# Kernel tuning notes

Hardware: AMD Instinct MI355X
Metric: run time of the kernel (lower is better)

The kernel has to match this reference:

```python
import jax, jax.numpy as jnp
import numpy as np

B, T, C = 8, 1024, 768
H, D = 12, 64  # num_heads, head_size; H*D == C
BLOCK = 1024


def setup_inputs() -> dict:
    key = jax.random.key(0)
    ks = jax.random.split(key, 6)
    s = C ** -0.5  # init scale akin to torch Linear default range
    x = jax.random.normal(ks[0], (B, T, C), dtype=jnp.float32)
    Wq = jax.random.normal(ks[1], (C, H, D), dtype=jnp.float32) * s
    Wk = jax.random.normal(ks[2], (C, H, D), dtype=jnp.float32) * s
    Wv = jax.random.normal(ks[3], (C, H, D), dtype=jnp.float32) * s
    Wp = jax.random.normal(ks[4], (C, C), dtype=jnp.float32) * s
    bp = jax.random.normal(ks[5], (C,), dtype=jnp.float32) * s
    return {"x": x, "Wq": Wq, "Wk": Wk, "Wv": Wv, "Wp": Wp, "bp": bp}


def reference(x, Wq, Wk, Wv, Wp, bp):
    # Fused equivalent of the per-head loop: project all heads at once.
    q = jnp.einsum('btc,chd->bhtd', x, Wq)  # [B,H,T,D]
    k = jnp.einsum('btc,chd->bhtd', x, Wk)
    v = jnp.einsum('btc,chd->bhtd', x, Wv)
    scale = D ** -0.5
    scores = jnp.einsum('bhtd,bhsd->bhts', q, k) * scale  # [B,H,T,T]
    causal = jnp.tril(jnp.ones((T, T), dtype=bool))       # tril mask (T <= block_size)
    scores = jnp.where(causal, scores, jnp.finfo(scores.dtype).min)
    att = jax.nn.softmax(scores, axis=-1)
    # dropout layers are identity in eval mode (deterministic reference)
    out = jnp.einsum('bhts,bhsd->bhtd', att, v)            # [B,H,T,D]
    out = out.transpose(0, 2, 1, 3).reshape(B, T, H * D)   # concat heads -> [B,T,C]
    return out @ Wp.T + bp  # output projection (torch Linear: y = x W^T + b)
```

## Files before the change

kernel.cpp:

```cpp
#include <hip/hip_runtime.h>

#define BB 8
#define TT 1024
#define CC 768
#define HH 12
#define DD 64

typedef float f32x4 __attribute__((ext_vector_type(4)));
typedef short s16x8 __attribute__((ext_vector_type(8)));

#define SCALE2 0.18033688011112042f

__device__ __forceinline__ unsigned short f2bf(float f) {
  unsigned u = __builtin_bit_cast(unsigned, f);
  u += 0x7fffu + ((u >> 16) & 1u);
  return (unsigned short)(u >> 16);
}

#define GLOAD_LDS16(gsrc, ldst)                                                     \
  __builtin_amdgcn_global_load_lds(                                                 \
      (const __attribute__((address_space(1))) void*)(gsrc),                        \
      (__attribute__((address_space(3))) void*)(ldst), 16, 0, 0)

__global__ __launch_bounds__(256) void cast_f32_bf16(const float* __restrict__ src,
                                                     unsigned short* __restrict__ dst,
                                                     int n4) {
  int i = blockIdx.x * 256 + threadIdx.x;
  if (i >= n4) return;
  float4 v = ((const float4*)src)[i];
  ushort4 o;
  o.x = f2bf(v.x); o.y = f2bf(v.y); o.z = f2bf(v.z); o.w = f2bf(v.w);
  ((ushort4*)dst)[i] = o;
}

__global__ __launch_bounds__(256) void transpose_w(const float* __restrict__ Wq,
                                                   const float* __restrict__ Wk,
                                                   const float* __restrict__ Wv,
                                                   unsigned short* __restrict__ WT) {
  __shared__ float tile[32][33];
  int bid = blockIdx.x;
  int which = bid / (24 * 24);
  int rem = bid % (24 * 24);
  int cb = (rem / 24) * 32, nb = (rem % 24) * 32;
  const float* W = (which == 0) ? Wq : (which == 1) ? Wk : Wv;
  int t = threadIdx.x;
  int j = t & 31, i0 = t >> 5;
  #pragma unroll
  for (int rr = 0; rr < 4; ++rr) {
    int i = i0 + rr * 8;
    tile[i][j] = W[(size_t)(cb + i) * CC + nb + j];
  }
  __syncthreads();
  #pragma unroll
  for (int rr = 0; rr < 4; ++rr) {
    int i = i0 + rr * 8;
    WT[(size_t)(which * CC + nb + i) * CC + cb + j] = f2bf(tile[j][i]);
  }
}

__device__ __forceinline__ void gemm_tile(const unsigned short* __restrict__ A,
                                          const unsigned short* __restrict__ BT,
                                          int m0, int n0,
                                          unsigned short* As, unsigned short* Bs,
                                          f32x4 acc[4][4]) {
  const int t = threadIdx.x, lane = t & 63, w = t >> 6;
  const int g = lane >> 4, c = lane & 15;
  const int wr = w >> 1, wc = w & 1;
  const int srow = lane >> 3;
  const int scol = (lane & 7) * 8;
  #pragma unroll 1
  for (int kt = 0; kt < CC; kt += 64) {
    __syncthreads();
    #pragma unroll
    for (int p = 0; p < 4; ++p) {
      int row = p * 32 + w * 8 + srow;
      GLOAD_LDS16(A + (size_t)(m0 + row) * CC + kt + scol, As + (p * 32 + w * 8) * 64);
      GLOAD_LDS16(BT + (size_t)(n0 + row) * CC + kt + scol, Bs + (p * 32 + w * 8) * 64);
    }
    __syncthreads();
    #pragma unroll
    for (int ks = 0; ks < 2; ++ks) {
      s16x8 a[4], b[4];
      #pragma unroll
      for (int i = 0; i < 4; ++i) {
        a[i] = *(const s16x8*)(As + (wr * 64 + i * 16 + c) * 64 + ks * 32 + g * 8);
        b[i] = *(const s16x8*)(Bs + (wc * 64 + i * 16 + c) * 64 + ks * 32 + g * 8);
      }
      #pragma unroll
      for (int i = 0; i < 4; ++i)
        #pragma unroll
        for (int j = 0; j < 4; ++j)
          acc[i][j] = __builtin_amdgcn_mfma_f32_16x16x32_bf16(a[i], b[j], acc[i][j], 0, 0, 0);
    }
  }
}

__global__ __launch_bounds__(256) void gemm_qkv(const unsigned short* __restrict__ xb,
                                                const unsigned short* __restrict__ WT,
                                                unsigned short* __restrict__ qb,
                                                unsigned short* __restrict__ kb,
                                                unsigned short* __restrict__ vT) {
  __shared__ unsigned short As[128 * 64], Bs[128 * 64];
  int bid = blockIdx.x;
  int bm = bid % 64, bn = bid / 64;
  int m0 = bm * 128, n0 = bn * 128;
  f32x4 acc[4][4];
  #pragma unroll
  for (int i = 0; i < 4; ++i)
    #pragma unroll
    for (int j = 0; j < 4; ++j)
      acc[i][j] = (f32x4){0.f, 0.f, 0.f, 0.f};
  gemm_tile(xb, WT, m0, n0, As, Bs, acc);

  const int t = threadIdx.x, lane = t & 63, w = t >> 6;
  const int g = lane >> 4, c = lane & 15;
  const int wr = w >> 1, wc = w & 1;
  #pragma unroll
  for (int i = 0; i < 4; ++i) {
    int mrow = m0 + wr * 64 + i * 16 + g * 4;
    int b = mrow >> 10, tt_ = mrow & 1023;
    #pragma unroll
    for (int j = 0; j < 4; ++j) {
      int nbv = n0 + wc * 64 + j * 16;
      int which = nbv / CC;
      int rm = nbv - which * CC;
      int h = rm >> 6, d0 = rm & 63;
      if (which == 2) {
        ushort4 pk;
        pk.x = f2bf(acc[i][j][0]); pk.y = f2bf(acc[i][j][1]);
        pk.z = f2bf(acc[i][j][2]); pk.w = f2bf(acc[i][j][3]);
        *(ushort4*)(vT + ((size_t)(b * HH + h) * DD + d0 + c) * TT + tt_) = pk;
      } else {
        float sc = which ? 1.0f : SCALE2;
        unsigned short* dst = (which ? kb : qb) +
                              ((size_t)(b * HH + h) * TT + tt_) * DD + d0 + c;
        dst[0]      = f2bf(acc[i][j][0] * sc);
        dst[DD]     = f2bf(acc[i][j][1] * sc);
        dst[2 * DD] = f2bf(acc[i][j][2] * sc);
        dst[3 * DD] = f2bf(acc[i][j][3] * sc);
      }
    }
  }
}

__global__ __launch_bounds__(256, 4) void attn(const unsigned short* __restrict__ qb,
                                               const unsigned short* __restrict__ kb,
                                               const unsigned short* __restrict__ vT,
                                               unsigned short* __restrict__ ao) {
  __shared__ unsigned short P[4][16 * 64];
  int bid = blockIdx.x;
  int sub = bid & 7, bh = bid >> 3;
  int b = bh / HH, h = bh % HH;
  int t = threadIdx.x, lane = t & 63, w = t >> 6;
  int g = lane >> 4, c = lane & 15;
  unsigned short* Pw = P[w];
  const unsigned short* Q = qb + (size_t)bh * TT * DD;
  const unsigned short* K = kb + (size_t)bh * TT * DD;
  const unsigned short* V = vT + (size_t)bh * DD * TT;
  int p = sub * 4 + w;

  #pragma unroll 1
  for (int half = 0; half < 2; ++half) {
    int strip = half ? (63 - p) : p;
    int q0 = strip * 16;

    s16x8 aq[2];
    #pragma unroll
    for (int ks = 0; ks < 2; ++ks)
      aq[ks] = *(const s16x8*)(Q + (size_t)(q0 + c) * DD + ks * 32 + g * 8);

    f32x4 acco[4];
    float mrow[4], lrow[4];
    #pragma unroll
    for (int nj = 0; nj < 4; ++nj) acco[nj] = (f32x4){0.f, 0.f, 0.f, 0.f};
    #pragma unroll
    for (int r = 0; r < 4; ++r) { mrow[r] = -1e30f; lrow[r] = 0.f; }

    int ntile = (q0 + 79) >> 6;
    #pragma unroll 1
    for (int kt = 0; kt < ntile; ++kt) {
      int s0 = kt * 64;
      f32x4 accs[4];
      #pragma unroll
      for (int nj = 0; nj < 4; ++nj) accs[nj] = (f32x4){0.f, 0.f, 0.f, 0.f};

      #pragma unroll
      for (int ks = 0; ks < 2; ++ks) {
        s16x8 bk[4];
        #pragma unroll
        for (int nj = 0; nj < 4; ++nj)
          bk[nj] = *(const s16x8*)(K + (size_t)(s0 + nj * 16 + c) * DD + ks * 32 + g * 8);
        #pragma unroll
        for (int nj = 0; nj < 4; ++nj)
          accs[nj] = __builtin_amdgcn_mfma_f32_16x16x32_bf16(aq[ks], bk[nj],
                                                             accs[nj], 0, 0, 0);
      }

      float nm[4], fs[4];
      bool diag = (kt == ntile - 1);
      if (diag) {
        #pragma unroll
        for (int r = 0; r < 4; ++r) {
          int trow = q0 + g * 4 + r;
          #pragma unroll
          for (int nj = 0; nj < 4; ++nj)
            if (s0 + nj * 16 + c > trow) accs[nj][r] = -1e30f;
        }
      }
      #pragma unroll
      for (int r = 0; r < 4; ++r) {
        float mx = fmaxf(fmaxf(accs[0][r], accs[1][r]), fmaxf(accs[2][r], accs[3][r]));
        mx = fmaxf(mx, __shfl_xor(mx, 1));
        mx = fmaxf(mx, __shfl_xor(mx, 2));
        mx = fmaxf(mx, __shfl_xor(mx, 4));
        mx = fmaxf(mx, __shfl_xor(mx, 8));
        float newm = fmaxf(mrow[r], mx);
        fs[r] = __builtin_amdgcn_exp2f(mrow[r] - newm);
        mrow[r] = newm;
        nm[r] = newm;
      }
      #pragma unroll
      for (int nj = 0; nj < 4; ++nj)
        #pragma unroll
        for (int r = 0; r < 4; ++r)
          accs[nj][r] = __builtin_amdgcn_exp2f(accs[nj][r] - nm[r]);
      #pragma unroll
      for (int r = 0; r < 4; ++r) {
        float s = (accs[0][r] + accs[1][r]) + (accs[2][r] + accs[3][r]);
        s += __shfl_xor(s, 1);
        s += __shfl_xor(s, 2);
        s += __shfl_xor(s, 4);
        s += __shfl_xor(s, 8);
        lrow[r] = lrow[r] * fs[r] + s;
      }
      #pragma unroll
      for (int nj = 0; nj < 4; ++nj)
        #pragma unroll
        for (int r = 0; r < 4; ++r) acco[nj][r] *= fs[r];

      #pragma unroll
      for (int nj = 0; nj < 4; ++nj)
        #pragma unroll
        for (int r = 0; r < 4; ++r) {
          int tr = g * 4 + r;
          Pw[(tr * 64 + nj * 16 + c) ^ ((tr & 7) << 3)] = f2bf(accs[nj][r]);
        }
      asm volatile("" ::: "memory");

      #pragma unroll
      for (int ks = 0; ks < 2; ++ks) {
        s16x8 bv[4];
        #pragma unroll
        for (int nj = 0; nj < 4; ++nj)
          bv[nj] = *(const s16x8*)(V + (size_t)(nj * 16 + c) * TT + s0 + ks * 32 + g * 8);
        s16x8 pa = *(const s16x8*)(Pw + ((c * 64 + ks * 32 + g * 8) ^ ((c & 7) << 3)));
        #pragma unroll
        for (int nj = 0; nj < 4; ++nj)
          acco[nj] = __builtin_amdgcn_mfma_f32_16x16x32_bf16(pa, bv[nj],
                                                             acco[nj], 0, 0, 0);
      }
      asm volatile("" ::: "memory");
    }

    #pragma unroll
    for (int r = 0; r < 4; ++r) {
      float inv = 1.0f / lrow[r];
      int trow = q0 + g * 4 + r;
      size_t rowb = ((size_t)b * TT + trow) * CC + h * DD;
      #pragma unroll
      for (int nj = 0; nj < 4; ++nj)
        ao[rowb + nj * 16 + c] = f2bf(acco[nj][r] * inv);
    }
  }
}

__global__ __launch_bounds__(256) void gemm_proj(const unsigned short* __restrict__ ao,
                                                 const unsigned short* __restrict__ WpB,
                                                 const float* __restrict__ bp,
                                                 float* __restrict__ out) {
  __shared__ unsigned short As[128 * 64], Bs[128 * 64];
  int bid = blockIdx.x;
  int bm = bid % 64, bn = bid / 64;
  int m0 = bm * 128, n0 = bn * 128;
  f32x4 acc[4][4];
  #pragma unroll
  for (int i = 0; i < 4; ++i)
    #pragma unroll
    for (int j = 0; j < 4; ++j)
      acc[i][j] = (f32x4){0.f, 0.f, 0.f, 0.f};
  gemm_tile(ao, WpB, m0, n0, As, Bs, acc);

  const int t = threadIdx.x, lane = t & 63, w = t >> 6;
  const int g = lane >> 4, c = lane & 15;
  const int wr = w >> 1, wc = w & 1;
  #pragma unroll
  for (int i = 0; i < 4; ++i) {
    int mrow = m0 + wr * 64 + i * 16 + g * 4;
    #pragma unroll
    for (int j = 0; j < 4; ++j) {
      int nn = n0 + wc * 64 + j * 16 + c;
      float bias = bp[nn];
      float* dst = out + (size_t)mrow * CC + nn;
      dst[0]        = acc[i][j][0] + bias;
      dst[CC]       = acc[i][j][1] + bias;
      dst[2 * CC]   = acc[i][j][2] + bias;
      dst[3 * CC]   = acc[i][j][3] + bias;
    }
  }
}

extern "C" void kernel_launch(void* const* d_in, const int* in_sizes, int n_in,
                              void* d_out, int out_size, void* d_ws, size_t ws_size,
                              hipStream_t stream) {
  (void)in_sizes; (void)n_in; (void)out_size; (void)ws_size;
  const float* x  = (const float*)d_in[0];
  const float* Wq = (const float*)d_in[1];
  const float* Wk = (const float*)d_in[2];
  const float* Wv = (const float*)d_in[3];
  const float* Wp = (const float*)d_in[4];
  const float* bp = (const float*)d_in[5];
  float* out = (float*)d_out;

  char* ws = (char*)d_ws;
  unsigned short* xb  = (unsigned short*)(ws);
  unsigned short* WT  = (unsigned short*)(ws + 12582912);
  unsigned short* WpB = (unsigned short*)(ws + 16121856);
  unsigned short* qb  = (unsigned short*)(ws + 17301504);
  unsigned short* kb  = (unsigned short*)(ws + 29884416);
  unsigned short* vT  = (unsigned short*)(ws + 42467328);
  unsigned short* aob = (unsigned short*)(ws + 55050240);

  cast_f32_bf16<<<6144, 256, 0, stream>>>(x, xb, 1572864);
  cast_f32_bf16<<<576, 256, 0, stream>>>(Wp, WpB, 147456);
  transpose_w<<<1728, 256, 0, stream>>>(Wq, Wk, Wv, WT);
  gemm_qkv<<<1152, 256, 0, stream>>>(xb, WT, qb, kb, vT);
  attn<<<768, 256, 0, stream>>>(qb, kb, vT, aob);
  gemm_proj<<<384, 256, 0, stream>>>(aob, WpB, bp, out);
}
```

Measured before the change: 286.5 us.

## Process both query strips together to share K/V loads and defer row-sum reduction

The attention kernel used to walk its two causal query strips one after the other. It now processes both in a single key-tile loop, so each K and V fragment loaded from global memory feeds both strips while the early strip is still active. The per-tile cross-lane shuffle reduction of the softmax row sum is replaced by per-lane partial sums that are reduced once at the end. It also issues V loads before the softmax so their latency is hidden, and double-buffers the P scratch in LDS. The cost is more live registers (two sets of accumulators and Q fragments), which may pressure the 4-blocks-per-CU occupancy target.

```diff
diff --git a/kernel.cpp b/kernel.cpp
--- a/kernel.cpp
+++ b/kernel.cpp
@@ -143,134 +143,183 @@
   }
 }
 
+__device__ __forceinline__ void softmax_tile(f32x4 accs[4], float m[4], float lp[4],
+                                             f32x4 acco[4], int q0, int s0, bool diag,
+                                             int g, int c, unsigned short* Pst) {
+  if (diag) {
+    #pragma unroll
+    for (int nj = 0; nj < 4; ++nj)
+      #pragma unroll
+      for (int r = 0; r < 4; ++r)
+        if (s0 + nj * 16 + c > q0 + g * 4 + r) accs[nj][r] = -1e30f;
+  }
+  float fs[4];
+  #pragma unroll
+  for (int r = 0; r < 4; ++r) {
+    float mx = fmaxf(fmaxf(accs[0][r], accs[1][r]), fmaxf(accs[2][r], accs[3][r]));
+    mx = fmaxf(mx, __shfl_xor(mx, 1));
+    mx = fmaxf(mx, __shfl_xor(mx, 2));
+    mx = fmaxf(mx, __shfl_xor(mx, 4));
+    mx = fmaxf(mx, __shfl_xor(mx, 8));
+    float newm = fmaxf(m[r], mx);
+    fs[r] = __builtin_amdgcn_exp2f(m[r] - newm);
+    m[r] = newm;
+  }
+  #pragma unroll
+  for (int nj = 0; nj < 4; ++nj)
+    #pragma unroll
+    for (int r = 0; r < 4; ++r)
+      accs[nj][r] = __builtin_amdgcn_exp2f(accs[nj][r] - m[r]);
+  #pragma unroll
+  for (int r = 0; r < 4; ++r) {
+    float s = (accs[0][r] + accs[1][r]) + (accs[2][r] + accs[3][r]);
+    lp[r] = lp[r] * fs[r] + s;
+    #pragma unroll
+    for (int nj = 0; nj < 4; ++nj) acco[nj][r] *= fs[r];
+  }
+  #pragma unroll
+  for (int nj = 0; nj < 4; ++nj)
+    #pragma unroll
+    for (int r = 0; r < 4; ++r) {
+      int tr = g * 4 + r;
+      Pst[(tr * 64 + nj * 16 + c) ^ ((tr & 7) << 3)] = f2bf(accs[nj][r]);
+    }
+}
+
 __global__ __launch_bounds__(256, 4) void attn(const unsigned short* __restrict__ qb,
                                                const unsigned short* __restrict__ kb,
                                                const unsigned short* __restrict__ vT,
                                                unsigned short* __restrict__ ao) {
-  __shared__ unsigned short P[4][16 * 64];
+  __shared__ unsigned short P[4][2][16 * 64];
   int bid = blockIdx.x;
   int sub = bid & 7, bh = bid >> 3;
   int b = bh / HH, h = bh % HH;
   int t = threadIdx.x, lane = t & 63, w = t >> 6;
   int g = lane >> 4, c = lane & 15;
-  unsigned short* Pw = P[w];
+  unsigned short* PA = P[w][0];
+  unsigned short* PB = P[w][1];
   const unsigned short* Q = qb + (size_t)bh * TT * DD;
   const unsigned short* K = kb + (size_t)bh * TT * DD;
   const unsigned short* V = vT + (size_t)bh * DD * TT;
   int p = sub * 4 + w;
+  int qA = p * 16, qB = (63 - p) * 16;
+  int ntA = (qA + 79) >> 6, ntB = (qB + 79) >> 6;
+
+  s16x8 aqA[2], aqB[2];
+  #pragma unroll
+  for (int ks = 0; ks < 2; ++ks) {
+    aqA[ks] = *(const s16x8*)(Q + (size_t)(qA + c) * DD + ks * 32 + g * 8);
+    aqB[ks] = *(const s16x8*)(Q + (size_t)(qB + c) * DD + ks * 32 + g * 8);
+  }
+
+  f32x4 accoA[4], accoB[4];
+  float mA[4], lA[4], mB[4], lB[4];
+  #pragma unroll
+  for (int nj = 0; nj < 4; ++nj) {
+    accoA[nj] = (f32x4){0.f, 0.f, 0.f, 0.f};
+    accoB[nj] = (f32x4){0.f, 0.f, 0.f, 0.f};
+  }
+  #pragma unroll
+  for (int r = 0; r < 4; ++r) {
+    mA[r] = -1e30f; lA[r] = 0.f;
+    mB[r] = -1e30f; lB[r] = 0.f;
+  }
 
   #pragma unroll 1
-  for (int half = 0; half < 2; ++half) {
-    int strip = half ? (63 - p) : p;
-    int q0 = strip * 16;
-
-    s16x8 aq[2];
-    #pragma unroll
-    for (int ks = 0; ks < 2; ++ks)
-      aq[ks] = *(const s16x8*)(Q + (size_t)(q0 + c) * DD + ks * 32 + g * 8);
-
-    f32x4 acco[4];
-    float mrow[4], lrow[4];
-    #pragma unroll
-    for (int nj = 0; nj < 4; ++nj) acco[nj] = (f32x4){0.f, 0.f, 0.f, 0.f};
-    #pragma unroll
-    for (int r = 0; r < 4; ++r) { mrow[r] = -1e30f; lrow[r] = 0.f; }
-
-    int ntile = (q0 + 79) >> 6;
-    #pragma unroll 1
-    for (int kt = 0; kt < ntile; ++kt) {
-      int s0 = kt * 64;
-      f32x4 accs[4];
-      #pragma unroll
-      for (int nj = 0; nj < 4; ++nj) accs[nj] = (f32x4){0.f, 0.f, 0.f, 0.f};
-
-      #pragma unroll
-      for (int ks = 0; ks < 2; ++ks) {
-        s16x8 bk[4];
+  for (int kt = 0; kt < ntB; ++kt) {
+    int s0 = kt * 64;
+    bool dual = (kt < ntA);
+    f32x4 accsA[4], accsB[4];
+    #pragma unroll
+    for (int nj = 0; nj < 4; ++nj) {
+      accsA[nj] = (f32x4){0.f, 0.f, 0.f, 0.f};
+      accsB[nj] = (f32x4){0.f, 0.f, 0.f, 0.f};
+    }
+
+    #pragma unroll
+    for (int ks = 0; ks < 2; ++ks) {
+      s16x8 bk[4];
+      #pragma unroll
+      for (int nj = 0; nj < 4; ++nj)
+        bk[nj] = *(const s16x8*)(K + (size_t)(s0 + nj * 16 + c) * DD + ks * 32 + g * 8);
+      #pragma unroll
+      for (int nj = 0; nj < 4; ++nj)
+        accsB[nj] = __builtin_amdgcn_mfma_f32_16x16x32_bf16(aqB[ks], bk[nj],
+                                                            accsB[nj], 0, 0, 0);
+      if (dual) {
         #pragma unroll
         for (int nj = 0; nj < 4; ++nj)
-          bk[nj] = *(const s16x8*)(K + (size_t)(s0 + nj * 16 + c) * DD + ks * 32 + g * 8);
+          accsA[nj] = __builtin_amdgcn_mfma_f32_16x16x32_bf16(aqA[ks], bk[nj],
+                                                              accsA[nj], 0, 0, 0);
+      }
+    }
+
+    s16x8 bv0[4], bv1[4];
+    #pragma unroll
+    for (int nj = 0; nj < 4; ++nj)
+      bv0[nj] = *(const s16x8*)(V + (size_t)(nj * 16 + c) * TT + s0 + g * 8);
+
+    if (dual) softmax_tile(accsA, mA, lA, accoA, qA, s0, kt == ntA - 1, g, c, PA);
+
+    #pragma unroll
+    for (int nj = 0; nj < 4; ++nj)
+      bv1[nj] = *(const s16x8*)(V + (size_t)(nj * 16 + c) * TT + s0 + 32 + g * 8);
+
+    softmax_tile(accsB, mB, lB, accoB, qB, s0, kt == ntB - 1, g, c, PB);
+    asm volatile("" ::: "memory");
+
+    {
+      s16x8 paB0 = *(const s16x8*)(PB + ((c * 64 + g * 8) ^ ((c & 7) << 3)));
+      s16x8 paB1 = *(const s16x8*)(PB + ((c * 64 + 32 + g * 8) ^ ((c & 7) << 3)));
+      #pragma unroll
+      for (int nj = 0; nj < 4; ++nj)
+        accoB[nj] = __builtin_amdgcn_mfma_f32_16x16x32_bf16(paB0, bv0[nj],
+                                                            accoB[nj], 0, 0, 0);
+      #pragma unroll
+      for (int nj = 0; nj < 4; ++nj)
+        accoB[nj] = __builtin_amdgcn_mfma_f32_16x16x32_bf16(paB1, bv1[nj],
+                                                            accoB[nj], 0, 0, 0);
+      if (dual) {
+        s16x8 paA0 = *(const s16x8*)(PA + ((c * 64 + g * 8) ^ ((c & 7) << 3)));
+        s16x8 paA1 = *(const s16x8*)(PA + ((c * 64 + 32 + g * 8) ^ ((c & 7) << 3)));
         #pragma unroll
         for (int nj = 0; nj < 4; ++nj)
-          accs[nj] = __builtin_amdgcn_mfma_f32_16x16x32_bf16(aq[ks], bk[nj],
-                                                             accs[nj], 0, 0, 0);
-      }
-
-      float nm[4], fs[4];
-      bool diag = (kt == ntile - 1);
-      if (diag) {
-        #pragma unroll
-        for (int r = 0; r < 4; ++r) {
-          int trow = q0 + g * 4 + r;
-          #pragma unroll
-          for (int nj = 0; nj < 4; ++nj)
-            if (s0 + nj * 16 + c > trow) accs[nj][r] = -1e30f;
-        }
-      }
-      #pragma unroll
-      for (int r = 0; r < 4; ++r) {
-        float mx = fmaxf(fmaxf(accs[0][r], accs[1][r]), fmaxf(accs[2][r], accs[3][r]));
-        mx = fmaxf(mx, __shfl_xor(mx, 1));
-        mx = fmaxf(mx, __shfl_xor(mx, 2));
-        mx = fmaxf(mx, __shfl_xor(mx, 4));
-        mx = fmaxf(mx, __shfl_xor(mx, 8));
-        float newm = fmaxf(mrow[r], mx);
-        fs[r] = __builtin_amdgcn_exp2f(mrow[r] - newm);
-        mrow[r] = newm;
-        nm[r] = newm;
-      }
-      #pragma unroll
-      for (int nj = 0; nj < 4; ++nj)
-        #pragma unroll
-        for (int r = 0; r < 4; ++r)
-          accs[nj][r] = __builtin_amdgcn_exp2f(accs[nj][r] - nm[r]);
-      #pragma unroll
-      for (int r = 0; r < 4; ++r) {
-        float s = (accs[0][r] + accs[1][r]) + (accs[2][r] + accs[3][r]);
-        s += __shfl_xor(s, 1);
-        s += __shfl_xor(s, 2);
-        s += __shfl_xor(s, 4);
-        s += __shfl_xor(s, 8);
-        lrow[r] = lrow[r] * fs[r] + s;
-      }
-      #pragma unroll
-      for (int nj = 0; nj < 4; ++nj)
-        #pragma unroll
-        for (int r = 0; r < 4; ++r) acco[nj][r] *= fs[r];
-
-      #pragma unroll
-      for (int nj = 0; nj < 4; ++nj)
-        #pragma unroll
-        for (int r = 0; r < 4; ++r) {
-          int tr = g * 4 + r;
-          Pw[(tr * 64 + nj * 16 + c) ^ ((tr & 7) << 3)] = f2bf(accs[nj][r]);
-        }
-      asm volatile("" ::: "memory");
-
-      #pragma unroll
-      for (int ks = 0; ks < 2; ++ks) {
-        s16x8 bv[4];
+          accoA[nj] = __builtin_amdgcn_mfma_f32_16x16x32_bf16(paA0, bv0[nj],
+                                                              accoA[nj], 0, 0, 0);
         #pragma unroll
         for (int nj = 0; nj < 4; ++nj)
-          bv[nj] = *(const s16x8*)(V + (size_t)(nj * 16 + c) * TT + s0 + ks * 32 + g * 8);
-        s16x8 pa = *(const s16x8*)(Pw + ((c * 64 + ks * 32 + g * 8) ^ ((c & 7) << 3)));
-        #pragma unroll
-        for (int nj = 0; nj < 4; ++nj)
-          acco[nj] = __builtin_amdgcn_mfma_f32_16x16x32_bf16(pa, bv[nj],
-                                                             acco[nj], 0, 0, 0);
+          accoA[nj] = __builtin_amdgcn_mfma_f32_16x16x32_bf16(paA1, bv1[nj],
+                                                              accoA[nj], 0, 0, 0);
       }
-      asm volatile("" ::: "memory");
-    }
-
-    #pragma unroll
-    for (int r = 0; r < 4; ++r) {
-      float inv = 1.0f / lrow[r];
-      int trow = q0 + g * 4 + r;
-      size_t rowb = ((size_t)b * TT + trow) * CC + h * DD;
-      #pragma unroll
-      for (int nj = 0; nj < 4; ++nj)
-        ao[rowb + nj * 16 + c] = f2bf(acco[nj][r] * inv);
-    }
+    }
+    asm volatile("" ::: "memory");
+  }
+
+  #pragma unroll
+  for (int r = 0; r < 4; ++r) {
+    float sA = lA[r];
+    sA += __shfl_xor(sA, 1);
+    sA += __shfl_xor(sA, 2);
+    sA += __shfl_xor(sA, 4);
+    sA += __shfl_xor(sA, 8);
+    float invA = 1.0f / sA;
+    int trA = qA + g * 4 + r;
+    size_t rowbA = ((size_t)b * TT + trA) * CC + h * DD;
+    #pragma unroll
+    for (int nj = 0; nj < 4; ++nj)
+      ao[rowbA + nj * 16 + c] = f2bf(accoA[nj][r] * invA);
+
+    float sB = lB[r];
+    sB += __shfl_xor(sB, 1);
+    sB += __shfl_xor(sB, 2);
+    sB += __shfl_xor(sB, 4);
+    sB += __shfl_xor(sB, 8);
+    float invB = 1.0f / sB;
+    int trB = qB + g * 4 + r;
+    size_t rowbB = ((size_t)b * TT + trB) * CC + h * DD;
+    #pragma unroll
+    for (int nj = 0; nj < 4; ++nj)
+      ao[rowbB + nj * 16 + c] = f2bf(accoB[nj][r] * invB);
   }
 }
 
```

After: 321.6 us. 1.12x slower.

## Prefetch K/V tiles in registers, defer row-sum reduction, remap blocks per XCD

Applied to the files above, without the earlier changes.

The attention loop now loads the next K tile and the current V tile into registers before the softmax, so global load latency overlaps with softmax math. The per-tile cross-lane shuffle reduction of the row sum is replaced by per-lane partial sums that are reduced once at the end. This is valid because the rescale factor is uniform across the row. Block indices are remapped so that all strips of a given batch-head land on the same XCD, aiming for better L2 reuse of K/V. Launch bounds drop to 2 blocks per SM to make room for the extra registers, which reduces occupancy.

```diff
diff --git a/kernel.cpp b/kernel.cpp
--- a/kernel.cpp
+++ b/kernel.cpp
@@ -143,13 +143,58 @@
   }
 }
 
-__global__ __launch_bounds__(256, 4) void attn(const unsigned short* __restrict__ qb,
+__device__ __forceinline__ void softmax_tile(f32x4 accs[4], float m[4], float lp[4],
+                                             f32x4 acco[4], int q0, int s0, bool diag,
+                                             int g, int c, unsigned short* Pst) {
+  if (diag) {
+    #pragma unroll
+    for (int nj = 0; nj < 4; ++nj)
+      #pragma unroll
+      for (int r = 0; r < 4; ++r)
+        if (s0 + nj * 16 + c > q0 + g * 4 + r) accs[nj][r] = -1e30f;
+  }
+  float fs[4];
+  #pragma unroll
+  for (int r = 0; r < 4; ++r) {
+    float mx = fmaxf(fmaxf(accs[0][r], accs[1][r]), fmaxf(accs[2][r], accs[3][r]));
+    mx = fmaxf(mx, __shfl_xor(mx, 1));
+    mx = fmaxf(mx, __shfl_xor(mx, 2));
+    mx = fmaxf(mx, __shfl_xor(mx, 4));
+    mx = fmaxf(mx, __shfl_xor(mx, 8));
+    float newm = fmaxf(m[r], mx);
+    fs[r] = __builtin_amdgcn_exp2f(m[r] - newm);
+    m[r] = newm;
+  }
+  #pragma unroll
+  for (int nj = 0; nj < 4; ++nj)
+    #pragma unroll
+    for (int r = 0; r < 4; ++r)
+      accs[nj][r] = __builtin_amdgcn_exp2f(accs[nj][r] - m[r]);
+  #pragma unroll
+  for (int r = 0; r < 4; ++r) {
+    float s = (accs[0][r] + accs[1][r]) + (accs[2][r] + accs[3][r]);
+    lp[r] = lp[r] * fs[r] + s;
+    #pragma unroll
+    for (int nj = 0; nj < 4; ++nj) acco[nj][r] *= fs[r];
+  }
+  #pragma unroll
+  for (int nj = 0; nj < 4; ++nj)
+    #pragma unroll
+    for (int r = 0; r < 4; ++r) {
+      int tr = g * 4 + r;
+      Pst[(tr * 64 + nj * 16 + c) ^ ((tr & 7) << 3)] = f2bf(accs[nj][r]);
+    }
+}
+
+__global__ __launch_bounds__(256, 2) void attn(const unsigned short* __restrict__ qb,
                                                const unsigned short* __restrict__ kb,
                                                const unsigned short* __restrict__ vT,
                                                unsigned short* __restrict__ ao) {
   __shared__ unsigned short P[4][16 * 64];
-  int bid = blockIdx.x;
-  int sub = bid & 7, bh = bid >> 3;
+  int bid0 = blockIdx.x;
+  int xcd = bid0 & 7, slot = bid0 >> 3;
+  int m12 = slot % 12, sub = slot / 12;
+  int bh = xcd * 12 + m12;
   int b = bh / HH, h = bh % HH;
   int t = threadIdx.x, lane = t & 63, w = t >> 6;
   int g = lane >> 4, c = lane & 15;
@@ -177,6 +222,14 @@
     for (int r = 0; r < 4; ++r) { mrow[r] = -1e30f; lrow[r] = 0.f; }
 
     int ntile = (q0 + 79) >> 6;
+
+    s16x8 bk[2][4];
+    #pragma unroll
+    for (int ks = 0; ks < 2; ++ks)
+      #pragma unroll
+      for (int nj = 0; nj < 4; ++nj)
+        bk[ks][nj] = *(const s16x8*)(K + (size_t)(nj * 16 + c) * DD + ks * 32 + g * 8);
+
     #pragma unroll 1
     for (int kt = 0; kt < ntile; ++kt) {
       int s0 = kt * 64;
@@ -185,78 +238,37 @@
       for (int nj = 0; nj < 4; ++nj) accs[nj] = (f32x4){0.f, 0.f, 0.f, 0.f};
 
       #pragma unroll
-      for (int ks = 0; ks < 2; ++ks) {
-        s16x8 bk[4];
+      for (int ks = 0; ks < 2; ++ks)
         #pragma unroll
         for (int nj = 0; nj < 4; ++nj)
-          bk[nj] = *(const s16x8*)(K + (size_t)(s0 + nj * 16 + c) * DD + ks * 32 + g * 8);
+          accs[nj] = __builtin_amdgcn_mfma_f32_16x16x32_bf16(aq[ks], bk[ks][nj],
+                                                             accs[nj], 0, 0, 0);
+
+      s16x8 bv[2][4];
+      #pragma unroll
+      for (int ks = 0; ks < 2; ++ks)
         #pragma unroll
         for (int nj = 0; nj < 4; ++nj)
-          accs[nj] = __builtin_amdgcn_mfma_f32_16x16x32_bf16(aq[ks], bk[nj],
-                                                             accs[nj], 0, 0, 0);
-      }
-
-      float nm[4], fs[4];
-      bool diag = (kt == ntile - 1);
-      if (diag) {
-        #pragma unroll
-        for (int r = 0; r < 4; ++r) {
-          int trow = q0 + g * 4 + r;
+          bv[ks][nj] = *(const s16x8*)(V + (size_t)(nj * 16 + c) * TT +
+                                       s0 + ks * 32 + g * 8);
+      if (kt + 1 < ntile) {
+        #pragma unroll
+        for (int ks = 0; ks < 2; ++ks)
           #pragma unroll
           for (int nj = 0; nj < 4; ++nj)
-            if (s0 + nj * 16 + c > trow) accs[nj][r] = -1e30f;
-        }
+            bk[ks][nj] = *(const s16x8*)(K + (size_t)(s0 + 64 + nj * 16 + c) * DD +
+                                         ks * 32 + g * 8);
       }
-      #pragma unroll
-      for (int r = 0; r < 4; ++r) {
-        float mx = fmaxf(fmaxf(accs[0][r], accs[1][r]), fmaxf(accs[2][r], accs[3][r]));
-        mx = fmaxf(mx, __shfl_xor(mx, 1));
-        mx = fmaxf(mx, __shfl_xor(mx, 2));
-        mx = fmaxf(mx, __shfl_xor(mx, 4));
-        mx = fmaxf(mx, __shfl_xor(mx, 8));
-        float newm = fmaxf(mrow[r], mx);
-        fs[r] = __builtin_amdgcn_exp2f(mrow[r] - newm);
-        mrow[r] = newm;
-        nm[r] = newm;
-      }
-      #pragma unroll
-      for (int nj = 0; nj < 4; ++nj)
-        #pragma unroll
-        for (int r = 0; r < 4; ++r)
-          accs[nj][r] = __builtin_amdgcn_exp2f(accs[nj][r] - nm[r]);
-      #pragma unroll
-      for (int r = 0; r < 4; ++r) {
-        float s = (accs[0][r] + accs[1][r]) + (accs[2][r] + accs[3][r]);
-        s += __shfl_xor(s, 1);
-        s += __shfl_xor(s, 2);
-        s += __shfl_xor(s, 4);
-        s += __shfl_xor(s, 8);
-        lrow[r] = lrow[r] * fs[r] + s;
-      }
-      #pragma unroll
-      for (int nj = 0; nj < 4; ++nj)
-        #pragma unroll
-        for (int r = 0; r < 4; ++r) acco[nj][r] *= fs[r];
-
-      #pragma unroll
-      for (int nj = 0; nj < 4; ++nj)
-        #pragma unroll
-        for (int r = 0; r < 4; ++r) {
-          int tr = g * 4 + r;
-          Pw[(tr * 64 + nj * 16 + c) ^ ((tr & 7) << 3)] = f2bf(accs[nj][r]);
-        }
+
+      softmax_tile(accs, mrow, lrow, acco, q0, s0, kt == ntile - 1, g, c, Pw);
       asm volatile("" ::: "memory");
 
       #pragma unroll
       for (int ks = 0; ks < 2; ++ks) {
-        s16x8 bv[4];
+        s16x8 pa = *(const s16x8*)(Pw + ((c * 64 + ks * 32 + g * 8) ^ ((c & 7) << 3)));
         #pragma unroll
         for (int nj = 0; nj < 4; ++nj)
-          bv[nj] = *(const s16x8*)(V + (size_t)(nj * 16 + c) * TT + s0 + ks * 32 + g * 8);
-        s16x8 pa = *(const s16x8*)(Pw + ((c * 64 + ks * 32 + g * 8) ^ ((c & 7) << 3)));
-        #pragma unroll
-        for (int nj = 0; nj < 4; ++nj)
-          acco[nj] = __builtin_amdgcn_mfma_f32_16x16x32_bf16(pa, bv[nj],
+          acco[nj] = __builtin_amdgcn_mfma_f32_16x16x32_bf16(pa, bv[ks][nj],
                                                              acco[nj], 0, 0, 0);
       }
       asm volatile("" ::: "memory");
@@ -264,7 +276,12 @@
 
     #pragma unroll
     for (int r = 0; r < 4; ++r) {
-      float inv = 1.0f / lrow[r];
+      float s = lrow[r];
+      s += __shfl_xor(s, 1);
+      s += __shfl_xor(s, 2);
+      s += __shfl_xor(s, 4);
+      s += __shfl_xor(s, 8);
+      float inv = 1.0f / s;
       int trow = q0 + g * 4 + r;
       size_t rowb = ((size_t)b * TT + trow) * CC + h * DD;
       #pragma unroll
```

Measured after the change: 270.0 us. 1.06x faster.
